# Optimization experiments

Measured on AMD Instinct MI355X. Metric: run time of the kernel, lower is better.

Reference implementation:

```python
import jax, jax.numpy as jnp
import numpy as np

B, T, D, H = 8, 2048, 2048, 128  # batch, seq_len, d_model, head_size
NEG = -1e9


def setup_inputs() -> dict:
    key = jax.random.key(0)
    k0, k1, k2, k3 = jax.random.split(key, 4)
    x = jax.random.normal(k0, (B, T, D), dtype=jnp.float32)
    s = 1.0 / np.sqrt(D)
    Wq = jax.random.normal(k1, (D, H), dtype=jnp.float32) * s
    Wk = jax.random.normal(k2, (D, H), dtype=jnp.float32) * s
    Wv = jax.random.normal(k3, (D, H), dtype=jnp.float32) * s
    return {"x": x, "Wq": Wq, "Wk": Wk, "Wv": Wv}


def reference(x, Wq, Wk, Wv):
    # projections: [B,T,H]
    q = jnp.einsum('btd,dh->bth', x, Wq)
    k = jnp.einsum('btd,dh->bth', x, Wk)
    v = jnp.einsum('btd,dh->bth', x, Wv)
    # NOTE: module multiplies by sqrt(head_size) (faithful to source)
    wei = jnp.einsum('bqh,bkh->bqk', q, k) * jnp.sqrt(jnp.float32(H))
    causal = jnp.tril(jnp.ones((T, T), dtype=bool))
    wei = jnp.where(causal, wei, jnp.float32(NEG))
    wei = jax.nn.softmax(wei, axis=-1)
    # dropout is identity (deterministic=True / rate=0)
    out = jnp.einsum('bqk,bkh->bqh', wei, v)
    return out
```

## Files before the change

### kernel.cpp

```cpp
#include <hip/hip_runtime.h>
#include <math.h>

#define B_ 8
#define T_ 2048
#define D_ 2048
#define H_ 128
#define M_ (B_ * T_)

typedef __bf16 bf16x8 __attribute__((ext_vector_type(8)));
typedef __bf16 bf16x4 __attribute__((ext_vector_type(4)));
typedef float f32x4 __attribute__((ext_vector_type(4)));

#define MFMA(a, b, c) __builtin_amdgcn_mfma_f32_16x16x32_bf16(a, b, c, 0, 0, 0)

#define QH_OFF 0
#define QL_OFF (1 * 2097152)
#define KH_OFF (2 * 2097152)
#define KL_OFF (3 * 2097152)
#define VT_OFF (4 * 2097152)
#define WTH_OFF (5 * 2097152)
#define WTL_OFF (WTH_OFF + 786432)

__global__ __launch_bounds__(256) void prep_kernel(
    const float* __restrict__ Wq, const float* __restrict__ Wk,
    const float* __restrict__ Wv, __bf16* __restrict__ wt_hi,
    __bf16* __restrict__ wt_lo) {
  const int z = blockIdx.y;
  const int k0 = blockIdx.x * 64;
  const float* W = z == 0 ? Wq : z == 1 ? Wk : Wv;
  __shared__ float tile[64][132];
  const int t = threadIdx.x;
#pragma unroll
  for (int it = 0; it < 8; ++it) {
    int f4 = it * 256 + t;
    int row = f4 >> 5, c = (f4 & 31) << 2;
    *(float4*)&tile[row][c] = *(const float4*)&W[(size_t)(k0 + row) * H_ + c];
  }
  __syncthreads();
  int n = t >> 1, kh = (t & 1) << 5;
  __bf16 h[32], l[32];
#pragma unroll
  for (int kk = 0; kk < 32; ++kk) {
    float x = tile[kh + kk][n];
    __bf16 hi = (__bf16)x;
    h[kk] = hi;
    l[kk] = (__bf16)(x - (float)hi);
  }
  size_t base = (size_t)(z * H_ + n) * D_ + k0 + kh;
#pragma unroll
  for (int c = 0; c < 4; ++c) {
    *(bf16x8*)&wt_hi[base + c * 8] = *(bf16x8*)&h[c * 8];
    *(bf16x8*)&wt_lo[base + c * 8] = *(bf16x8*)&l[c * 8];
  }
}

#define WSTR 36
#define XSTR 72

__global__ __launch_bounds__(512, 4) void proj_kernel(
    const float* __restrict__ X, const __bf16* __restrict__ wt_hi,
    const __bf16* __restrict__ wt_lo, __bf16* __restrict__ qh,
    __bf16* __restrict__ ql, __bf16* __restrict__ kh,
    __bf16* __restrict__ kl, __bf16* __restrict__ vt) {
  __shared__ __align__(16) __bf16 Wh[192 * WSTR];
  __shared__ __align__(16) __bf16 Wl[192 * WSTR];
  __shared__ __align__(16) __bf16 Xs[64 * XSTR];
  const int t = threadIdx.x;
  const int wv = t >> 6, lane = t & 63;
  const int l15 = lane & 15, quad = lane >> 4, q8 = quad * 8;
  const int bi = blockIdx.x;
  const int m0 = (bi >> 1) * 64;
  const int nbase = (bi & 1) * 192;
  const int wr = wv >> 2, wc = wv & 3;
  const int xm = t >> 3, xk = (t & 7) << 2;
  const float* xgp = X + (size_t)(m0 + xm) * D_ + xk;
  const __bf16* wsrc[3];
  __bf16* wdst[3];
#pragma unroll
  for (int p = 0; p < 3; ++p) {
    int c = t + (p << 9);
    int sel = c >= 768;
    int cr = sel ? c - 768 : c;
    int r = cr >> 2, o = (c & 3) << 3;
    wsrc[p] = (sel ? wt_lo : wt_hi) + (size_t)(nbase + r) * D_ + o;
    wdst[p] = (sel ? Wl : Wh) + r * WSTR + o;
  }
  f32x4 acc[2][3] = {};
  float4 xr = *(const float4*)xgp;
  bf16x8 wreg[3];
#pragma unroll
  for (int p = 0; p < 3; ++p) wreg[p] = *(const bf16x8*)wsrc[p];
  for (int ks = 0; ks < 64; ++ks) {
    __syncthreads();
    {
      __bf16 h0 = (__bf16)xr.x, h1 = (__bf16)xr.y, h2 = (__bf16)xr.z,
             h3 = (__bf16)xr.w;
      bf16x4 hv = {h0, h1, h2, h3};
      bf16x4 lv = {(__bf16)(xr.x - (float)h0), (__bf16)(xr.y - (float)h1),
                   (__bf16)(xr.z - (float)h2), (__bf16)(xr.w - (float)h3)};
      *(bf16x4*)&Xs[xm * XSTR + xk] = hv;
      *(bf16x4*)&Xs[xm * XSTR + 32 + xk] = lv;
    }
#pragma unroll
    for (int p = 0; p < 3; ++p) {
      bf16x4 a, b;
#pragma unroll
      for (int j = 0; j < 4; ++j) {
        a[j] = wreg[p][j];
        b[j] = wreg[p][j + 4];
      }
      *(bf16x4*)(wdst[p]) = a;
      *(bf16x4*)(wdst[p] + 4) = b;
    }
    if (ks < 63) {
      const int ko = (ks + 1) << 5;
      xr = *(const float4*)(xgp + ko);
#pragma unroll
      for (int p = 0; p < 3; ++p)
        wreg[p] = *(const bf16x8*)(wsrc[p] + ko);
    }
    __syncthreads();
    bf16x8 ah[2], al[2];
#pragma unroll
    for (int mg = 0; mg < 2; ++mg) {
      ah[mg] = *(bf16x8*)&Xs[(wr * 32 + mg * 16 + l15) * XSTR + q8];
      al[mg] = *(bf16x8*)&Xs[(wr * 32 + mg * 16 + l15) * XSTR + 32 + q8];
    }
#pragma unroll
    for (int nt = 0; nt < 3; ++nt) {
      const int n = wc * 48 + nt * 16 + l15;
      bf16x4 b0 = *(bf16x4*)&Wh[n * WSTR + q8];
      bf16x4 b1 = *(bf16x4*)&Wh[n * WSTR + q8 + 4];
      bf16x4 b2 = *(bf16x4*)&Wl[n * WSTR + q8];
      bf16x4 b3 = *(bf16x4*)&Wl[n * WSTR + q8 + 4];
      bf16x8 bh, bl;
#pragma unroll
      for (int j = 0; j < 4; ++j) {
        bh[j] = b0[j];
        bh[j + 4] = b1[j];
        bl[j] = b2[j];
        bl[j + 4] = b3[j];
      }
#pragma unroll
      for (int mg = 0; mg < 2; ++mg) {
        acc[mg][nt] = MFMA(ah[mg], bh, acc[mg][nt]);
        acc[mg][nt] = MFMA(al[mg], bh, acc[mg][nt]);
        acc[mg][nt] = MFMA(ah[mg], bl, acc[mg][nt]);
      }
    }
  }
#pragma unroll
  for (int nt = 0; nt < 3; ++nt) {
    int ncb = nbase + wc * 48 + nt * 16;
    int z = ncb >> 7;
    int h = (ncb & 127) + l15;
#pragma unroll
    for (int mg = 0; mg < 2; ++mg) {
      int r0 = m0 + wr * 32 + mg * 16 + quad * 4;
      if (z == 2) {
        int b = m0 >> 11;
        int tt0 = (m0 & 2047) + wr * 32 + mg * 16 + quad * 4;
        bf16x4 pv = {(__bf16)acc[mg][nt][0], (__bf16)acc[mg][nt][1],
                     (__bf16)acc[mg][nt][2], (__bf16)acc[mg][nt][3]};
        *(bf16x4*)&vt[(size_t)(b * H_ + h) * T_ + tt0] = pv;
      } else {
        __bf16* dh = z == 0 ? qh : kh;
        __bf16* dl = z == 0 ? ql : kl;
#pragma unroll
        for (int reg = 0; reg < 4; ++reg) {
          float v = acc[mg][nt][reg];
          __bf16 hi = (__bf16)v;
          dh[(size_t)(r0 + reg) * H_ + h] = hi;
          dl[(size_t)(r0 + reg) * H_ + h] = (__bf16)(v - (float)hi);
        }
      }
    }
  }
}

__global__ __launch_bounds__(512, 2) void attn_kernel(
    const __bf16* __restrict__ qh, const __bf16* __restrict__ qlo,
    const __bf16* __restrict__ kh, const __bf16* __restrict__ klo,
    const __bf16* __restrict__ vt, float* __restrict__ out) {
  const int t = threadIdx.x;
  const int wv = t >> 6, st = wv >> 2, cw = wv & 3;
  const int lane = t & 63, l15 = lane & 15, quad = lane >> 4;
  const int j = blockIdx.x, b = j & 7, pi = j >> 3;
  const int qlidx = (st == 0) ? pi : 63 - pi;
  const int t0 = qlidx * 32;
  const int nkt = (qlidx >> 1) + 1;
  __shared__ __align__(16) __bf16 Pbuf[8][32 * 72];
  __shared__ __align__(16) float Obuf[2][32 * 132];
  __shared__ float mlb[2][4][32], llb[2][4][32];
  const size_t qrow0 = (size_t)b * T_ + t0;
  bf16x8 qfh[2][4], qfl[2][4];
#pragma unroll
  for (int mg = 0; mg < 2; ++mg)
#pragma unroll
    for (int ds = 0; ds < 4; ++ds) {
      size_t off = (qrow0 + mg * 16 + l15) * H_ + ds * 32 + quad * 8;
      qfh[mg][ds] = *(const bf16x8*)(qh + off);
      qfl[mg][ds] = *(const bf16x8*)(qlo + off);
    }
  f32x4 O[2][8] = {};
  float ms[2][4], ls[2][4];
#pragma unroll
  for (int mg = 0; mg < 2; ++mg)
#pragma unroll
    for (int reg = 0; reg < 4; ++reg) {
      ms[mg][reg] = -INFINITY;
      ls[mg][reg] = 0.f;
    }
  const __bf16* vtb = vt + (size_t)b * H_ * T_;
  const float scale = 11.313708498984761f;
  for (int kt_i = cw; kt_i < nkt; kt_i += 4) {
    const int kt = kt_i * 64;
    f32x4 S[2][4] = {};
#pragma unroll
    for (int ds = 0; ds < 4; ++ds)
#pragma unroll
      for (int ct = 0; ct < 4; ++ct) {
        size_t koff =
            ((size_t)b * T_ + kt + ct * 16 + l15) * H_ + ds * 32 + quad * 8;
        bf16x8 bh = *(const bf16x8*)(kh + koff);
        bf16x8 bl = *(const bf16x8*)(klo + koff);
#pragma unroll
        for (int mg = 0; mg < 2; ++mg) {
          S[mg][ct] = MFMA(qfh[mg][ds], bh, S[mg][ct]);
          S[mg][ct] = MFMA(qfl[mg][ds], bh, S[mg][ct]);
          S[mg][ct] = MFMA(qfh[mg][ds], bl, S[mg][ct]);
        }
      }
    const bool diag = (kt_i == nkt - 1);
#pragma unroll
    for (int mg = 0; mg < 2; ++mg)
#pragma unroll
      for (int ct = 0; ct < 4; ++ct)
#pragma unroll
        for (int reg = 0; reg < 4; ++reg) {
          float s = S[mg][ct][reg] * scale;
          if (diag && (kt + ct * 16 + l15 > t0 + mg * 16 + quad * 4 + reg))
            s = -1e30f;
          S[mg][ct][reg] = s;
        }
    float al_[2][4];
#pragma unroll
    for (int mg = 0; mg < 2; ++mg)
#pragma unroll
      for (int reg = 0; reg < 4; ++reg) {
        float r = fmaxf(fmaxf(S[mg][0][reg], S[mg][1][reg]),
                        fmaxf(S[mg][2][reg], S[mg][3][reg]));
        r = fmaxf(r, __shfl_xor(r, 1));
        r = fmaxf(r, __shfl_xor(r, 2));
        r = fmaxf(r, __shfl_xor(r, 4));
        r = fmaxf(r, __shfl_xor(r, 8));
        float mn = fmaxf(ms[mg][reg], r);
        float a = __expf(ms[mg][reg] - mn);
        ms[mg][reg] = mn;
        float ps = 0.f;
#pragma unroll
        for (int ct = 0; ct < 4; ++ct) {
          float p = __expf(S[mg][ct][reg] - mn);
          S[mg][ct][reg] = p;
          ps += p;
        }
        ps += __shfl_xor(ps, 1);
        ps += __shfl_xor(ps, 2);
        ps += __shfl_xor(ps, 4);
        ps += __shfl_xor(ps, 8);
        ls[mg][reg] = ls[mg][reg] * a + ps;
        al_[mg][reg] = a;
      }
#pragma unroll
    for (int mg = 0; mg < 2; ++mg)
#pragma unroll
      for (int ht = 0; ht < 8; ++ht)
#pragma unroll
        for (int reg = 0; reg < 4; ++reg) O[mg][ht][reg] *= al_[mg][reg];
#pragma unroll
    for (int mg = 0; mg < 2; ++mg)
#pragma unroll
      for (int ct = 0; ct < 4; ++ct)
#pragma unroll
        for (int reg = 0; reg < 4; ++reg)
          Pbuf[wv][(mg * 16 + quad * 4 + reg) * 72 + ct * 16 + l15] =
              (__bf16)S[mg][ct][reg];
#pragma unroll
    for (int ks = 0; ks < 2; ++ks) {
      bf16x8 pf0 = *(bf16x8*)&Pbuf[wv][(l15)*72 + ks * 32 + quad * 8];
      bf16x8 pf1 = *(bf16x8*)&Pbuf[wv][(16 + l15) * 72 + ks * 32 + quad * 8];
#pragma unroll
      for (int ht = 0; ht < 8; ++ht) {
        bf16x8 vf = *(const bf16x8*)&vtb[(size_t)(ht * 16 + l15) * T_ + kt +
                                         ks * 32 + quad * 8];
        O[0][ht] = MFMA(pf0, vf, O[0][ht]);
        O[1][ht] = MFMA(pf1, vf, O[1][ht]);
      }
    }
  }
  if (l15 == 0) {
#pragma unroll
    for (int mg = 0; mg < 2; ++mg)
#pragma unroll
      for (int reg = 0; reg < 4; ++reg) {
        mlb[st][cw][mg * 16 + quad * 4 + reg] = ms[mg][reg];
        llb[st][cw][mg * 16 + quad * 4 + reg] = ls[mg][reg];
      }
  }
  for (int i = t; i < 2 * 32 * 132; i += 512) ((float*)Obuf)[i] = 0.f;
  __syncthreads();
  float aw[2][4];
#pragma unroll
  for (int mg = 0; mg < 2; ++mg)
#pragma unroll
    for (int reg = 0; reg < 4; ++reg) {
      int row = mg * 16 + quad * 4 + reg;
      float M = fmaxf(fmaxf(mlb[st][0][row], mlb[st][1][row]),
                      fmaxf(mlb[st][2][row], mlb[st][3][row]));
      float L = 0.f;
#pragma unroll
      for (int w = 0; w < 4; ++w)
        L += llb[st][w][row] * __expf(mlb[st][w][row] - M);
      aw[mg][reg] = __expf(ms[mg][reg] - M) / L;
    }
#pragma unroll
  for (int mg = 0; mg < 2; ++mg)
#pragma unroll
    for (int ht = 0; ht < 8; ++ht)
#pragma unroll
      for (int reg = 0; reg < 4; ++reg)
        atomicAdd(&Obuf[st][(mg * 16 + quad * 4 + reg) * 132 + ht * 16 + l15],
                  O[mg][ht][reg] * aw[mg][reg]);
  __syncthreads();
  {
    const int stw = t >> 8, tt = t & 255;
    const int qlw = (stw == 0) ? pi : 63 - pi;
    const size_t obase = ((size_t)b * T_ + qlw * 32) * H_;
#pragma unroll
    for (int i = 0; i < 4; ++i) {
      int f4 = i * 256 + tt;
      int row = f4 >> 5, c = (f4 & 31) << 2;
      *(float4*)&out[obase + (size_t)row * H_ + c] =
          *(float4*)&Obuf[stw][row * 132 + c];
    }
  }
}

extern "C" void kernel_launch(void* const* d_in, const int* in_sizes, int n_in,
                              void* d_out, int out_size, void* d_ws, size_t ws_size,
                              hipStream_t stream) {
  const float* x = (const float*)d_in[0];
  const float* Wq = (const float*)d_in[1];
  const float* Wk = (const float*)d_in[2];
  const float* Wv = (const float*)d_in[3];
  __bf16* ws = (__bf16*)d_ws;
  float* out = (float*)d_out;
  prep_kernel<<<dim3(32, 3), 256, 0, stream>>>(Wq, Wk, Wv, ws + WTH_OFF,
                                               ws + WTL_OFF);
  proj_kernel<<<512, 512, 0, stream>>>(x, ws + WTH_OFF, ws + WTL_OFF,
                                       ws + QH_OFF, ws + QL_OFF, ws + KH_OFF,
                                       ws + KL_OFF, ws + VT_OFF);
  attn_kernel<<<256, 512, 0, stream>>>(ws + QH_OFF, ws + QL_OFF, ws + KH_OFF,
                                       ws + KL_OFF, ws + VT_OFF, out);
}
```

Before: 377.4 us.

## Load projection weight fragments directly from global into registers, bypassing LDS

The projection kernel no longer stages the hi/lo bf16 weight tiles through shared memory. Each lane loads its MFMA B-operand fragments straight from global memory into double-buffered registers, using a two-step unrolled macro to ping-pong the buffers. This removes the LDS writes, LDS reads and repacking for W, and shrinks shared memory use. In exchange, each wave makes redundant global or L2 loads of the weights that were shared across waves before, and register pressure rises.

```diff
diff --git a/kernel.cpp b/kernel.cpp
--- a/kernel.cpp
+++ b/kernel.cpp
@@ -54,16 +54,48 @@
   }
 }
 
-#define WSTR 36
 #define XSTR 72
+
+#define PROJ_STEP(KS, CH, CL, NH, NL)                                     \
+  {                                                                       \
+    __syncthreads();                                                      \
+    {                                                                     \
+      __bf16 h0 = (__bf16)xr.x, h1 = (__bf16)xr.y, h2 = (__bf16)xr.z,     \
+             h3 = (__bf16)xr.w;                                           \
+      bf16x4 hv = {h0, h1, h2, h3};                                       \
+      bf16x4 lv = {(__bf16)(xr.x - (float)h0), (__bf16)(xr.y - (float)h1),\
+                   (__bf16)(xr.z - (float)h2), (__bf16)(xr.w - (float)h3)};\
+      *(bf16x4*)&Xs[xm * XSTR + xk] = hv;                                 \
+      *(bf16x4*)&Xs[xm * XSTR + 32 + xk] = lv;                            \
+    }                                                                     \
+    if ((KS) < 63) {                                                      \
+      const int ko = ((KS) + 1) << 5;                                     \
+      xr = *(const float4*)(xgp + ko);                                    \
+      _Pragma("unroll") for (int nt = 0; nt < 3; ++nt) {                  \
+        NH[nt] = *(const bf16x8*)(wph[nt] + ko);                          \
+        NL[nt] = *(const bf16x8*)(wpl[nt] + ko);                          \
+      }                                                                   \
+    }                                                                     \
+    __syncthreads();                                                      \
+    bf16x8 ah[2], al[2];                                                  \
+    _Pragma("unroll") for (int mg = 0; mg < 2; ++mg) {                    \
+      ah[mg] = *(bf16x8*)&Xs[(wr * 32 + mg * 16 + l15) * XSTR + q8];      \
+      al[mg] = *(bf16x8*)&Xs[(wr * 32 + mg * 16 + l15) * XSTR + 32 + q8]; \
+    }                                                                     \
+    _Pragma("unroll") for (int nt = 0; nt < 3; ++nt) {                    \
+      _Pragma("unroll") for (int mg = 0; mg < 2; ++mg) {                  \
+        acc[mg][nt] = MFMA(ah[mg], CH[nt], acc[mg][nt]);                  \
+        acc[mg][nt] = MFMA(al[mg], CH[nt], acc[mg][nt]);                  \
+        acc[mg][nt] = MFMA(ah[mg], CL[nt], acc[mg][nt]);                  \
+      }                                                                   \
+    }                                                                     \
+  }
 
 __global__ __launch_bounds__(512, 4) void proj_kernel(
     const float* __restrict__ X, const __bf16* __restrict__ wt_hi,
     const __bf16* __restrict__ wt_lo, __bf16* __restrict__ qh,
     __bf16* __restrict__ ql, __bf16* __restrict__ kh,
     __bf16* __restrict__ kl, __bf16* __restrict__ vt) {
-  __shared__ __align__(16) __bf16 Wh[192 * WSTR];
-  __shared__ __align__(16) __bf16 Wl[192 * WSTR];
   __shared__ __align__(16) __bf16 Xs[64 * XSTR];
   const int t = threadIdx.x;
   const int wv = t >> 6, lane = t & 63;
@@ -74,80 +106,25 @@
   const int wr = wv >> 2, wc = wv & 3;
   const int xm = t >> 3, xk = (t & 7) << 2;
   const float* xgp = X + (size_t)(m0 + xm) * D_ + xk;
-  const __bf16* wsrc[3];
-  __bf16* wdst[3];
-#pragma unroll
-  for (int p = 0; p < 3; ++p) {
-    int c = t + (p << 9);
-    int sel = c >= 768;
-    int cr = sel ? c - 768 : c;
-    int r = cr >> 2, o = (c & 3) << 3;
-    wsrc[p] = (sel ? wt_lo : wt_hi) + (size_t)(nbase + r) * D_ + o;
-    wdst[p] = (sel ? Wl : Wh) + r * WSTR + o;
+  const __bf16* wph[3];
+  const __bf16* wpl[3];
+#pragma unroll
+  for (int nt = 0; nt < 3; ++nt) {
+    size_t ro = (size_t)(nbase + wc * 48 + nt * 16 + l15) * D_ + q8;
+    wph[nt] = wt_hi + ro;
+    wpl[nt] = wt_lo + ro;
   }
   f32x4 acc[2][3] = {};
   float4 xr = *(const float4*)xgp;
-  bf16x8 wreg[3];
-#pragma unroll
-  for (int p = 0; p < 3; ++p) wreg[p] = *(const bf16x8*)wsrc[p];
-  for (int ks = 0; ks < 64; ++ks) {
-    __syncthreads();
-    {
-      __bf16 h0 = (__bf16)xr.x, h1 = (__bf16)xr.y, h2 = (__bf16)xr.z,
-             h3 = (__bf16)xr.w;
-      bf16x4 hv = {h0, h1, h2, h3};
-      bf16x4 lv = {(__bf16)(xr.x - (float)h0), (__bf16)(xr.y - (float)h1),
-                   (__bf16)(xr.z - (float)h2), (__bf16)(xr.w - (float)h3)};
-      *(bf16x4*)&Xs[xm * XSTR + xk] = hv;
-      *(bf16x4*)&Xs[xm * XSTR + 32 + xk] = lv;
-    }
-#pragma unroll
-    for (int p = 0; p < 3; ++p) {
-      bf16x4 a, b;
-#pragma unroll
-      for (int j = 0; j < 4; ++j) {
-        a[j] = wreg[p][j];
-        b[j] = wreg[p][j + 4];
-      }
-      *(bf16x4*)(wdst[p]) = a;
-      *(bf16x4*)(wdst[p] + 4) = b;
-    }
-    if (ks < 63) {
-      const int ko = (ks + 1) << 5;
-      xr = *(const float4*)(xgp + ko);
-#pragma unroll
-      for (int p = 0; p < 3; ++p)
-        wreg[p] = *(const bf16x8*)(wsrc[p] + ko);
-    }
-    __syncthreads();
-    bf16x8 ah[2], al[2];
-#pragma unroll
-    for (int mg = 0; mg < 2; ++mg) {
-      ah[mg] = *(bf16x8*)&Xs[(wr * 32 + mg * 16 + l15) * XSTR + q8];
-      al[mg] = *(bf16x8*)&Xs[(wr * 32 + mg * 16 + l15) * XSTR + 32 + q8];
-    }
-#pragma unroll
-    for (int nt = 0; nt < 3; ++nt) {
-      const int n = wc * 48 + nt * 16 + l15;
-      bf16x4 b0 = *(bf16x4*)&Wh[n * WSTR + q8];
-      bf16x4 b1 = *(bf16x4*)&Wh[n * WSTR + q8 + 4];
-      bf16x4 b2 = *(bf16x4*)&Wl[n * WSTR + q8];
-      bf16x4 b3 = *(bf16x4*)&Wl[n * WSTR + q8 + 4];
-      bf16x8 bh, bl;
-#pragma unroll
-      for (int j = 0; j < 4; ++j) {
-        bh[j] = b0[j];
-        bh[j + 4] = b1[j];
-        bl[j] = b2[j];
-        bl[j + 4] = b3[j];
-      }
-#pragma unroll
-      for (int mg = 0; mg < 2; ++mg) {
-        acc[mg][nt] = MFMA(ah[mg], bh, acc[mg][nt]);
-        acc[mg][nt] = MFMA(al[mg], bh, acc[mg][nt]);
-        acc[mg][nt] = MFMA(ah[mg], bl, acc[mg][nt]);
-      }
-    }
+  bf16x8 wha[3], wla[3], whb[3], wlb[3];
+#pragma unroll
+  for (int nt = 0; nt < 3; ++nt) {
+    wha[nt] = *(const bf16x8*)(wph[nt]);
+    wla[nt] = *(const bf16x8*)(wpl[nt]);
+  }
+  for (int ks2 = 0; ks2 < 64; ks2 += 2) {
+    PROJ_STEP(ks2, wha, wla, whb, wlb);
+    PROJ_STEP(ks2 + 1, whb, wlb, wha, wla);
   }
 #pragma unroll
   for (int nt = 0; nt < 3; ++nt) {
```

New measurement: 489.1 us. 29.6% more time.
